# Optimization experiments

Measured on AMD Instinct MI355X. Metric: run time of the kernel, lower is better.

The kernel has to match this reference:

```python
import jax, jax.numpy as jnp
import numpy as np

SEQ, BATCH, HIDDEN = 2048, 2, 2048
NUM_HEADS = 16
HEAD_DIM = HIDDEN // NUM_HEADS  # 128


def setup_inputs() -> dict:
    key = jax.random.key(0)
    k1, k2, k3, k4, k5 = jax.random.split(key, 5)
    scale = 1.0 / np.sqrt(HIDDEN)
    return {
        "hidden_states": jax.random.normal(k1, (SEQ, BATCH, HIDDEN), dtype=jnp.float32),
        "w_qkv": jax.random.normal(k2, (3 * HIDDEN, HIDDEN), dtype=jnp.float32) * scale,
        "b_qkv": jax.random.normal(k3, (3 * HIDDEN,), dtype=jnp.float32) * 0.01,
        "w_dense": jax.random.normal(k4, (HIDDEN, HIDDEN), dtype=jnp.float32) * scale,
        "b_dense": jax.random.normal(k5, (HIDDEN,), dtype=jnp.float32) * 0.01,
    }


def reference(hidden_states, w_qkv, b_qkv, w_dense, b_dense):
    s, b, H = hidden_states.shape
    nh, d = NUM_HEADS, HEAD_DIM
    norm_factor = jnp.asarray(np.sqrt(d), dtype=hidden_states.dtype)

    # QKV projection: [s, b, 3H] -> [s, b, nh, 3d] -> chunk into q, k, v
    mixed = hidden_states @ w_qkv.T + b_qkv
    mixed = mixed.reshape(s, b, nh, 3 * d)
    q, k, v = jnp.split(mixed, 3, axis=-1)  # each [s, b, nh, d]

    # Causal scaled dot-product attention, materializing [b, nh, sq, sk]
    scores = jnp.einsum("sbhd,tbhd->bhst", q, k) / norm_factor
    causal = jnp.tril(jnp.ones((s, s), dtype=bool))  # [sq, sk]
    scores = jnp.where(causal[None, None, :, :], scores, jnp.asarray(-10000.0, scores.dtype))
    probs = jax.nn.softmax(scores, axis=-1)

    # Context: [s, b, nh, d] -> [s, b, H]
    ctx = jnp.einsum("bhst,tbhd->sbhd", probs, v).reshape(s, b, H)

    # Output projection
    return ctx @ w_dense.T + b_dense
```

## Files before the change

### kernel.cpp

```cpp
#include <hip/hip_runtime.h>
#include <stdint.h>
#include <stddef.h>

#define SEQ   2048
#define BATCH 2
#define HID   2048
#define NH    16
#define HD    128
#define MTOT  (SEQ*BATCH)
#define NQKV  (3*HID)
#define KDIM  HID
#define LOG2E 1.4426950408889634f

#define BK64    64
#define NT64    (KDIM/BK64)

typedef short  bf16x8 __attribute__((ext_vector_type(8)));
typedef float  f32x4  __attribute__((ext_vector_type(4)));

__device__ __forceinline__ unsigned short f2bf(float f) {
  union { float f; uint32_t u; } a; a.f = f;
  uint32_t r = a.u + 0x7fffu + ((a.u >> 16) & 1u);
  return (unsigned short)(r >> 16);
}

__device__ __forceinline__ f32x4 mfma16(bf16x8 a, bf16x8 b, f32x4 c) {
  return __builtin_amdgcn_mfma_f32_16x16x32_bf16(a, b, c, 0, 0, 0);
}

__device__ __forceinline__ void gl_lds16(const unsigned short* g, unsigned short* l) {
  __builtin_amdgcn_global_load_lds(
      (const __attribute__((address_space(1))) void*)g,
      (__attribute__((address_space(3))) void*)l, 16, 0, 0);
}

__global__ void cvt_f32_bf16(const float* __restrict__ in,
                             unsigned short* __restrict__ out, int n4) {
  int i = blockIdx.x * blockDim.x + threadIdx.x;
  int stride = gridDim.x * blockDim.x;
  for (; i < n4; i += stride) {
    float4 f = reinterpret_cast<const float4*>(in)[i];
    ushort4 o;
    o.x = f2bf(f.x); o.y = f2bf(f.y); o.z = f2bf(f.z); o.w = f2bf(f.w);
    reinterpret_cast<ushort4*>(out)[i] = o;
  }
}

__global__ __launch_bounds__(256) void transpose_v(
    const unsigned short* __restrict__ V, unsigned short* __restrict__ Vt) {
  __shared__ unsigned short tile[64][72];
  const int t  = threadIdx.x;
  const int bh = blockIdx.z;
  const int s0 = blockIdx.x * 64;
  const int d0 = blockIdx.y * 64;
  const size_t vb = (size_t)bh * SEQ * HD;
  const size_t tb = (size_t)bh * HD * SEQ;
#pragma unroll
  for (int p = 0; p < 2; ++p) {
    int r = p * 32 + (t >> 3);
    *(uint4*)&tile[r][(t & 7) * 8] =
        *(const uint4*)&V[vb + (size_t)(s0 + r) * HD + d0 + (t & 7) * 8];
  }
  __syncthreads();
#pragma unroll
  for (int p = 0; p < 2; ++p) {
    int dr = p * 32 + (t >> 3);
    int sc = (t & 7) * 8;
    unsigned short tmp[8];
#pragma unroll
    for (int e = 0; e < 8; ++e) tmp[e] = tile[sc + e][dr];
    *(uint4*)&Vt[tb + (size_t)(d0 + dr) * SEQ + s0 + sc] = *(const uint4*)tmp;
  }
}


#define G8_SB()  asm volatile("s_barrier" ::: "memory")
#define G8_LGKM() do { asm volatile("s_waitcnt lgkmcnt(0)" ::: "memory");     \
                       __builtin_amdgcn_sched_barrier(0); } while (0)

#define G8_RDA(G) do {                                                        \
    p0 = *(const bf16x8*)&sb[abase + (2*(G)    ) * 1024 + ga0];               \
    p1 = *(const bf16x8*)&sb[abase + (2*(G)    ) * 1024 + ga1];               \
    p2 = *(const bf16x8*)&sb[abase + (2*(G) + 1) * 1024 + ga0];               \
    p3 = *(const bf16x8*)&sb[abase + (2*(G) + 1) * 1024 + ga1];               \
  } while (0)

#define G8_MFMA(G) do {                                                       \
    __builtin_amdgcn_s_setprio(1);                                            \
    _Pragma("unroll")                                                         \
    for (int n_ = 0; n_ < 4; ++n_) {                                          \
      acc[2*(G)][n_]     = mfma16(p0, bq0[n_], acc[2*(G)][n_]);               \
      acc[2*(G)][n_]     = mfma16(p1, bq1[n_], acc[2*(G)][n_]);               \
      acc[2*(G) + 1][n_] = mfma16(p2, bq0[n_], acc[2*(G) + 1][n_]);           \
      acc[2*(G) + 1][n_] = mfma16(p3, bq1[n_], acc[2*(G) + 1][n_]);           \
    }                                                                         \
    __builtin_amdgcn_sched_barrier(0);                                        \
    __builtin_amdgcn_s_setprio(0);                                            \
  } while (0)

#define G8_STA(R) gl_lds16(Asrc + (size_t)(R) * KDIM + koff,                  \
                           &db[((R) + w * 8) * 64])
#define G8_STB(R) gl_lds16(Bsrc + (size_t)(R) * KDIM + koff,                  \
                           &db[16384 + ((R) + w * 8) * 64])

#define G8_TILE(DOSTAGE, VM1, VM3) do {                                       \
    bf16x8 bq0[4], bq1[4], p0, p1, p2, p3;                                    \
                                                       \
    _Pragma("unroll")                                                         \
    for (int n_ = 0; n_ < 4; ++n_) {                                          \
      bq0[n_] = *(const bf16x8*)&sb[bbase + n_ * 1024 + ga0];                 \
      bq1[n_] = *(const bf16x8*)&sb[bbase + n_ * 1024 + ga1];                 \
    }                                                                         \
    G8_RDA(0);                                                                \
    if (DOSTAGE) { G8_STB(0); G8_STB(64); }                                   \
    G8_SB(); G8_LGKM();                                                       \
    G8_MFMA(0);                                                               \
    G8_SB();                                                                  \
                                                       \
    G8_RDA(1);                                                                \
    if (DOSTAGE) { G8_STB(128); G8_STB(192); }                                \
    asm volatile("s_waitcnt " VM1 ::: "memory");                              \
    G8_SB(); G8_LGKM();                                                       \
    G8_MFMA(1);                                                               \
    G8_SB();                                                                  \
                                                       \
    G8_RDA(2);                                                                \
    if (DOSTAGE) { G8_STA(0); G8_STA(128); }                                  \
    G8_SB(); G8_LGKM();                                                       \
    G8_MFMA(2);                                                               \
    G8_SB();                                                                  \
                                                       \
    G8_RDA(3);                                                                \
    if (DOSTAGE) { G8_STA(64); G8_STA(192); }                                 \
    asm volatile("s_waitcnt " VM3 ::: "memory");                              \
    G8_SB(); G8_LGKM();                                                       \
    G8_MFMA(3);                                                               \
    G8_SB();                                                                  \
  } while (0)

__global__ __launch_bounds__(512, 2) void qkv_gemm(
    const unsigned short* __restrict__ A,
    const unsigned short* __restrict__ B,
    const float* __restrict__ bias,
    unsigned short* __restrict__ Qo,
    unsigned short* __restrict__ Ko,
    unsigned short* __restrict__ Vo)
{
  __shared__ unsigned short smb[2 * 32768];
  const int id  = blockIdx.x;
  const int swz = (id & 7) * 48 + (id >> 3);
  const int m0 = (swz / 24) * 256, n0 = (swz % 24) * 256;
  const int t = threadIdx.x, l = t & 63, w = t >> 6;
  const int wm = w >> 2, wn = w & 3;
  const int fr = l & 15, fg = l >> 4;
  const int abase = (wm * 128 + fr) * 64;
  const int bbase = 16384 + (wn * 64 + fr) * 64;
  const int ga0 = ((fg     ) ^ (fr & 7)) * 8;
  const int ga1 = ((fg + 4 ) ^ (fr & 7)) * 8;
  const int srcrow = w * 8 + (l >> 3);
  const int sgr    = ((l & 7) ^ (l >> 3)) * 8;
  const unsigned short* Asrc = A + (size_t)(m0 + srcrow) * KDIM + sgr;
  const unsigned short* Bsrc = B + (size_t)(n0 + srcrow) * KDIM + sgr;
  f32x4 acc[8][4] = {};

  {
    unsigned short* db = smb;
    size_t koff = 0;
    G8_STB(0); G8_STB(64); G8_STB(128); G8_STB(192);
    G8_STA(0); G8_STA(128); G8_STA(64); G8_STA(192);
  }
  asm volatile("s_waitcnt vmcnt(2)" ::: "memory");
  asm volatile("s_barrier" ::: "memory");

#pragma unroll 1
  for (int kt = 0; kt < NT64 - 1; ++kt) {
    const unsigned short* sb = &smb[(kt & 1) * 32768];
    unsigned short* db = &smb[((kt + 1) & 1) * 32768];
    size_t koff = (size_t)(kt + 1) * BK64;
    G8_TILE(1, "vmcnt(4)", "vmcnt(2)");
  }
  {
    const unsigned short* sb = &smb[((NT64 - 1) & 1) * 32768];
    unsigned short* db = smb;
    size_t koff = 0; (void)koff;
    G8_TILE(0, "vmcnt(0)", "vmcnt(0)");
  }

#pragma unroll
  for (int n = 0; n < 4; ++n) {
    int ncol = n0 + wn * 64 + n * 16 + fr;
    float bv = bias[ncol];
    int head = ncol / 384;
    int rem  = ncol - head * 384;
    int wi   = rem >> 7;
    int d    = rem & 127;
    unsigned short* dst = (wi == 0) ? Qo : ((wi == 1) ? Ko : Vo);
#pragma unroll
    for (int m = 0; m < 8; ++m) {
#pragma unroll
      for (int j = 0; j < 4; ++j) {
        int r = m0 + wm * 128 + m * 16 + fg * 4 + j;
        int s = r >> 1, bb = r & 1;
        float val = acc[m][n][j] + bv;
        if (wi == 0) val *= 0.08838834764831845f;
        dst[(((size_t)(bb * NH + head)) * SEQ + s) * HD + d] = f2bf(val);
      }
    }
  }
}


#define GEMM_PRE()                                                            \
  const int t = threadIdx.x, l = t & 63, w = t >> 6;                          \
  const int wm = w >> 1, wn = w & 1;                                          \
  const int fr = l & 15, fg = l >> 4;                                         \
  const int fx = fr & 7;                                                      \
  const int srow = l >> 3;                                                    \
  const int sgr  = ((l & 7) ^ srow) * 8;                                      \
  const unsigned short* Aw = A + (size_t)(m0 + w * 32 + srow) * KDIM + sgr;   \
  const unsigned short* Bw = B + (size_t)(n0 + w * 16 + srow) * KDIM + sgr;   \
  unsigned short* smb = &sm[0][0];                                            \
  const int a0 = (wm * 64 + fr) * 64 + ((fg ^ fx) * 8);                       \
  const int a1 = (wm * 64 + fr) * 64 + (((4 + fg) ^ fx) * 8);                 \
  const int b0 = 16384 + (wn * 64 + fr) * 64 + ((fg ^ fx) * 8);               \
  const int b1 = 16384 + (wn * 64 + fr) * 64 + (((4 + fg) ^ fx) * 8);         \
  f32x4 acc[4][4] = {};

#define STAGE_AB(KT) do {                                                     \
    unsigned short* dst = &smb[((KT) % 3) * 24576];                           \
    const unsigned short* ap = Aw + (size_t)(KT) * BK64;                      \
    gl_lds16(ap,                    &dst[(w * 4 + 0) * 512]);                 \
    gl_lds16(ap + 8  * KDIM,        &dst[(w * 4 + 1) * 512]);                 \
    gl_lds16(ap + 16 * KDIM,        &dst[(w * 4 + 2) * 512]);                 \
    gl_lds16(ap + 24 * KDIM,        &dst[(w * 4 + 3) * 512]);                 \
    const unsigned short* bp = Bw + (size_t)(KT) * BK64;                      \
    gl_lds16(bp,                    &dst[16384 + (w * 2 + 0) * 512]);         \
    gl_lds16(bp + 8 * KDIM,         &dst[16384 + (w * 2 + 1) * 512]);         \
  } while (0)

#define GEMM_BODY(KT, VM, DOSTAGE) do {                                       \
    const unsigned short* sb = &smb[((KT) % 3) * 24576];                      \
    if (DOSTAGE) STAGE_AB((KT) + 2);                                          \
    bf16x8 af0[4], af1[4], bg0[4], bg1[4];                                    \
    _Pragma("unroll")                                                         \
    for (int m_ = 0; m_ < 4; ++m_) {                                          \
      af0[m_] = *(const bf16x8*)&sb[a0 + m_ * 1024];                          \
      af1[m_] = *(const bf16x8*)&sb[a1 + m_ * 1024];                          \
    }                                                                         \
    _Pragma("unroll")                                                         \
    for (int n_ = 0; n_ < 4; ++n_) {                                          \
      bg0[n_] = *(const bf16x8*)&sb[b0 + n_ * 1024];                          \
      bg1[n_] = *(const bf16x8*)&sb[b1 + n_ * 1024];                          \
    }                                                                         \
    asm volatile("s_waitcnt vmcnt(" #VM ")" ::: "memory");                    \
    asm volatile("s_barrier" ::: "memory");                                   \
    asm volatile("s_waitcnt lgkmcnt(0)" ::: "memory");                        \
    __builtin_amdgcn_sched_barrier(0);                                        \
    __builtin_amdgcn_s_setprio(1);                                            \
    _Pragma("unroll")                                                         \
    for (int m_ = 0; m_ < 4; ++m_)                                            \
      _Pragma("unroll")                                                       \
      for (int n_ = 0; n_ < 4; ++n_)                                          \
        acc[m_][n_] = mfma16(af0[m_], bg0[n_], acc[m_][n_]);                  \
    _Pragma("unroll")                                                         \
    for (int m_ = 0; m_ < 4; ++m_)                                            \
      _Pragma("unroll")                                                       \
      for (int n_ = 0; n_ < 4; ++n_)                                          \
        acc[m_][n_] = mfma16(af1[m_], bg1[n_], acc[m_][n_]);                  \
    __builtin_amdgcn_sched_barrier(0);                                        \
    __builtin_amdgcn_s_setprio(0);                                            \
    asm volatile("s_barrier" ::: "memory");                                   \
  } while (0)

#define GEMM_MAIN()                                                           \
  STAGE_AB(0); STAGE_AB(1);                                                   \
  asm volatile("s_waitcnt vmcnt(6)" ::: "memory");                            \
  asm volatile("s_barrier" ::: "memory");                                     \
  _Pragma("unroll 1")                                                         \
  for (int kt = 0; kt < NT64 - 2; ++kt)                                       \
    GEMM_BODY(kt, 6, 1);                                                      \
  GEMM_BODY(NT64 - 2, 0, 0);                                                  \
  GEMM_BODY(NT64 - 1, 0, 0);

__global__ __launch_bounds__(512, 1) void dense_gemm(
    const unsigned short* __restrict__ A,
    const unsigned short* __restrict__ B,
    const float* __restrict__ bias,
    float* __restrict__ out)
{
  __shared__ unsigned short sm[3][24576];
  int id  = blockIdx.x;
  int swz = (id & 7) * (gridDim.x >> 3) + (id >> 3);
  const int m0 = (swz / 16) * 256, n0 = (swz % 16) * 128;
  GEMM_PRE();
  GEMM_MAIN();

  const int g4 = fg * 4;
#pragma unroll
  for (int n = 0; n < 4; ++n) {
    int ncol = n0 + wn * 64 + n * 16 + fr;
    float bv = bias[ncol];
#pragma unroll
    for (int m = 0; m < 4; ++m) {
#pragma unroll
      for (int j = 0; j < 4; ++j) {
        int r = m0 + wm * 64 + m * 16 + g4 + j;
        out[(size_t)r * HID + ncol] = acc[m][n][j] + bv;
      }
    }
  }
}

__global__ __launch_bounds__(256, 2) void attn_fwd(
    const unsigned short* __restrict__ Q,
    const unsigned short* __restrict__ K,
    const unsigned short* __restrict__ Vt,
    unsigned short* __restrict__ ctx)
{
  __shared__ unsigned short Ksh[2][64 * 128];
  __shared__ unsigned short Vsh[2][128 * 64];
  __shared__ unsigned short Psh[4][16 * 72];
  const int t = threadIdx.x, l = t & 63, w = t >> 6;
  int nwg = gridDim.x * gridDim.y;
  int id  = blockIdx.y * gridDim.x + blockIdx.x;
  int swz = (id & 7) * (nwg >> 3) + (id >> 3);
  const int pair = swz & 15;
  const int bh   = swz >> 4;
  const int qtA = pair, qtB = 31 - pair;
  const int fr = l & 15, fg = l >> 4;
  const size_t base  = (size_t)bh * SEQ * HD;
  const size_t vbase = (size_t)bh * HD * SEQ;

#define STAGE(BUF, KT) do {                                                   \
    const unsigned short* Kt_ = K + base + (size_t)((KT) * 64) * HD;          \
    _Pragma("unroll")                                                         \
    for (int i_ = 0; i_ < 4; ++i_) {                                          \
      int ch_  = w * 4 + i_;                                                  \
      int row_ = ch_ * 4 + (l >> 4);                                          \
      int c16_ = (l & 15) ^ (row_ & 7);                                       \
      gl_lds16(Kt_ + (size_t)row_ * HD + c16_ * 8, &Ksh[BUF][ch_ * 512]);     \
    }                                                                         \
    const unsigned short* Vg_ = Vt + vbase + (KT) * 64;                       \
    _Pragma("unroll")                                                         \
    for (int i_ = 0; i_ < 4; ++i_) {                                          \
      int ch_  = w * 4 + i_;                                                  \
      int row_ = ch_ * 8 + (l >> 3);                                          \
      int c16_ = (l & 7) ^ (row_ & 7);                                        \
      gl_lds16(Vg_ + (size_t)row_ * SEQ + c16_ * 8, &Vsh[BUF][ch_ * 512]);    \
    }                                                                         \
  } while (0)

#define COMPUTE_TILE(QF, OACC, MROW, LROW, QT) do {                           \
    f32x4 sacc[4] = {};                                                       \
    _Pragma("unroll")                                                         \
    for (int c_ = 0; c_ < 4; ++c_) {                                          \
      _Pragma("unroll")                                                       \
      for (int n_ = 0; n_ < 4; ++n_) {                                        \
        int krow = n_ * 16 + fr;                                              \
        int g_   = (c_ * 4 + fg) ^ (krow & 7);                                \
        bf16x8 kf = *(const bf16x8*)&Ksh[buf][krow * 128 + g_ * 8];           \
        sacc[n_] = mfma16(QF[c_], kf, sacc[n_]);                              \
      }                                                                       \
    }                                                                         \
    if (kt == (QT)) {                                                         \
      _Pragma("unroll")                                                       \
      for (int n_ = 0; n_ < 4; ++n_)                                          \
        _Pragma("unroll")                                                     \
        for (int j_ = 0; j_ < 4; ++j_)                                        \
          if (n_ * 16 + fr > w * 16 + fg * 4 + j_) sacc[n_][j_] = -1e30f;     \
    }                                                                         \
    float tm_[4];                                                             \
    _Pragma("unroll")                                                         \
    for (int j_ = 0; j_ < 4; ++j_) {                                          \
      float v0 = fmaxf(fmaxf(sacc[0][j_], sacc[1][j_]),                       \
                       fmaxf(sacc[2][j_], sacc[3][j_]));                      \
      v0 = fmaxf(v0, __shfl_xor(v0, 1));                                      \
      v0 = fmaxf(v0, __shfl_xor(v0, 2));                                      \
      v0 = fmaxf(v0, __shfl_xor(v0, 4));                                      \
      v0 = fmaxf(v0, __shfl_xor(v0, 8));                                      \
      tm_[j_] = v0;                                                           \
    }                                                                         \
    float sc_[4], ps_[4];                                                     \
    _Pragma("unroll")                                                         \
    for (int j_ = 0; j_ < 4; ++j_) {                                          \
      float mn_ = fmaxf(MROW[j_], tm_[j_]);                                   \
      sc_[j_] = exp2f((MROW[j_] - mn_) * LOG2E);                              \
      MROW[j_] = mn_;                                                         \
      ps_[j_] = 0.f;                                                          \
    }                                                                         \
    _Pragma("unroll")                                                         \
    for (int n_ = 0; n_ < 4; ++n_)                                            \
      _Pragma("unroll")                                                       \
      for (int j_ = 0; j_ < 4; ++j_) {                                        \
        float p_ = exp2f((sacc[n_][j_] - MROW[j_]) * LOG2E);                  \
        sacc[n_][j_] = p_;                                                    \
        ps_[j_] += p_;                                                        \
      }                                                                       \
    _Pragma("unroll")                                                         \
    for (int j_ = 0; j_ < 4; ++j_) {                                          \
      float s_ = ps_[j_];                                                     \
      s_ += __shfl_xor(s_, 1);                                                \
      s_ += __shfl_xor(s_, 2);                                                \
      s_ += __shfl_xor(s_, 4);                                                \
      s_ += __shfl_xor(s_, 8);                                                \
      LROW[j_] = LROW[j_] * sc_[j_] + s_;                                     \
    }                                                                         \
    _Pragma("unroll")                                                         \
    for (int n_ = 0; n_ < 8; ++n_)                                            \
      _Pragma("unroll")                                                       \
      for (int j_ = 0; j_ < 4; ++j_)                                          \
        OACC[n_][j_] *= sc_[j_];                                              \
    _Pragma("unroll")                                                         \
    for (int n_ = 0; n_ < 4; ++n_)                                            \
      _Pragma("unroll")                                                       \
      for (int j_ = 0; j_ < 4; ++j_)                                          \
        Psh[w][(fg * 4 + j_) * 72 + n_ * 16 + fr] = f2bf(sacc[n_][j_]);       \
    _Pragma("unroll")                                                         \
    for (int ks_ = 0; ks_ < 2; ++ks_) {                                       \
      bf16x8 pf = *(const bf16x8*)&Psh[w][fr * 72 + ks_ * 32 + fg * 8];       \
      _Pragma("unroll")                                                       \
      for (int n_ = 0; n_ < 8; ++n_) {                                        \
        int vrow = n_ * 16 + fr;                                              \
        int g_   = (ks_ * 4 + fg) ^ (vrow & 7);                               \
        bf16x8 vf = *(const bf16x8*)&Vsh[buf][vrow * 64 + g_ * 8];            \
        OACC[n_] = mfma16(pf, vf, OACC[n_]);                                  \
      }                                                                       \
    }                                                                         \
  } while (0)

  bf16x8 qfA[4], qfB[4];
  {
    const unsigned short* qpA = Q + base + (size_t)(qtA * 64 + w * 16 + fr) * HD + fg * 8;
    const unsigned short* qpB = Q + base + (size_t)(qtB * 64 + w * 16 + fr) * HD + fg * 8;
#pragma unroll
    for (int c = 0; c < 4; ++c) {
      qfA[c] = *(const bf16x8*)(qpA + c * 32);
      qfB[c] = *(const bf16x8*)(qpB + c * 32);
    }
  }
  f32x4 oaccA[8] = {}, oaccB[8] = {};
  float mA[4] = {-1e30f, -1e30f, -1e30f, -1e30f};
  float mB[4] = {-1e30f, -1e30f, -1e30f, -1e30f};
  float lA[4] = {0.f, 0.f, 0.f, 0.f};
  float lB[4] = {0.f, 0.f, 0.f, 0.f};

  STAGE(0, 0);
  __syncthreads();
  int buf = 0;
  for (int kt = 0; kt <= qtB; ++kt) {
    if (kt < qtB) STAGE(buf ^ 1, kt + 1);
    COMPUTE_TILE(qfB, oaccB, mB, lB, qtB);
    if (kt <= qtA) COMPUTE_TILE(qfA, oaccA, mA, lA, qtA);
    __syncthreads();
    buf ^= 1;
  }

  const int bb = bh >> 4, h = bh & 15;
#define WRITE_CTX(OACC, LROW, QT) do {                                        \
    _Pragma("unroll")                                                         \
    for (int n_ = 0; n_ < 8; ++n_)                                            \
      _Pragma("unroll")                                                       \
      for (int j_ = 0; j_ < 4; ++j_) {                                        \
        int qrow = (QT) * 64 + w * 16 + fg * 4 + j_;                          \
        float val = OACC[n_][j_] / LROW[j_];                                  \
        ctx[((size_t)(qrow * BATCH + bb)) * HID + h * HD + n_ * 16 + fr] =    \
            f2bf(val);                                                        \
      }                                                                       \
  } while (0)
  WRITE_CTX(oaccA, lA, qtA);
  WRITE_CTX(oaccB, lB, qtB);
#undef STAGE
#undef COMPUTE_TILE
#undef WRITE_CTX
}

extern "C" void kernel_launch(void* const* d_in, const int* in_sizes, int n_in,
                              void* d_out, int out_size, void* d_ws, size_t ws_size,
                              hipStream_t stream) {
  const float* hs      = (const float*)d_in[0];
  const float* w_qkv   = (const float*)d_in[1];
  const float* b_qkv   = (const float*)d_in[2];
  const float* w_dense = (const float*)d_in[3];
  const float* b_dense = (const float*)d_in[4];
  float* out = (float*)d_out;

  unsigned short* hsb = (unsigned short*)d_ws;
  unsigned short* wqb = hsb + (size_t)MTOT * HID;
  unsigned short* wdb = wqb + (size_t)NQKV * HID;
  unsigned short* q   = wdb + (size_t)HID * HID;
  unsigned short* k   = q   + (size_t)MTOT * HID;
  unsigned short* v   = k   + (size_t)MTOT * HID;
  unsigned short* ctx = v   + (size_t)MTOT * HID;
  unsigned short* vt  = hsb;

  cvt_f32_bf16<<<2048, 256, 0, stream>>>(hs,      hsb, (MTOT * HID) / 4);
  cvt_f32_bf16<<<2048, 256, 0, stream>>>(w_qkv,   wqb, (NQKV * HID) / 4);
  cvt_f32_bf16<<<1024, 256, 0, stream>>>(w_dense, wdb, (HID * HID) / 4);

  qkv_gemm<<<dim3((MTOT / 256) * (NQKV / 256)), 512, 0, stream>>>(hsb, wqb, b_qkv, q, k, v);
  transpose_v<<<dim3(SEQ / 64, HD / 64, BATCH * NH), 256, 0, stream>>>(v, vt);
  attn_fwd<<<dim3(16, 32), 256, 0, stream>>>(q, k, vt, ctx);
  dense_gemm<<<dim3((MTOT / 256) * (HID / 128)), 512, 0, stream>>>(ctx, wdb, b_dense, out);
}
```

Baseline: 285.4 us.

## Retile QKV GEMM to 256x192 blocks and merge conversion kernels

The QKV GEMM tile shrinks from 256x256 to 256x192. The grid grows from 384 to 512 blocks, which matches the CU count better (256 CUs with 2 blocks each) and avoids a partial wave. LDS staging, the swizzle and the per-wave MFMA loops are adjusted so each wave covers 48 columns, and the global-to-LDS stage ordering is rebalanced. The three f32-to-bf16 conversion launches are merged into one kernel to cut launch overhead. The trade-off is lower arithmetic intensity per block and changed vmcnt accounting in the pipeline.

After: 275.0 us. 1.04x faster.

```diff
diff --git a/kernel.cpp b/kernel.cpp
--- a/kernel.cpp
+++ b/kernel.cpp
@@ -34,15 +34,21 @@
       (__attribute__((address_space(3))) void*)l, 16, 0, 0);
 }
 
-__global__ void cvt_f32_bf16(const float* __restrict__ in,
-                             unsigned short* __restrict__ out, int n4) {
+__global__ void cvt3_f32_bf16(const float* __restrict__ a, unsigned short* __restrict__ oa, int na,
+                              const float* __restrict__ b, unsigned short* __restrict__ ob, int nb,
+                              const float* __restrict__ c, unsigned short* __restrict__ oc, int nc) {
   int i = blockIdx.x * blockDim.x + threadIdx.x;
   int stride = gridDim.x * blockDim.x;
-  for (; i < n4; i += stride) {
-    float4 f = reinterpret_cast<const float4*>(in)[i];
+  int ntot = na + nb + nc;
+  for (; i < ntot; i += stride) {
+    const float* src; unsigned short* dst; int j;
+    if (i < na)           { src = a; dst = oa; j = i; }
+    else if (i < na + nb) { src = b; dst = ob; j = i - na; }
+    else                  { src = c; dst = oc; j = i - na - nb; }
+    float4 f = reinterpret_cast<const float4*>(src)[j];
     ushort4 o;
     o.x = f2bf(f.x); o.y = f2bf(f.y); o.z = f2bf(f.z); o.w = f2bf(f.w);
-    reinterpret_cast<ushort4*>(out)[i] = o;
+    reinterpret_cast<ushort4*>(dst)[j] = o;
   }
 }
 
@@ -74,6 +80,8 @@
 }
 
 
+#define QBUFS 28672
+
 #define G8_SB()  asm volatile("s_barrier" ::: "memory")
 #define G8_LGKM() do { asm volatile("s_waitcnt lgkmcnt(0)" ::: "memory");     \
                        __builtin_amdgcn_sched_barrier(0); } while (0)
@@ -88,7 +96,7 @@
 #define G8_MFMA(G) do {                                                       \
     __builtin_amdgcn_s_setprio(1);                                            \
     _Pragma("unroll")                                                         \
-    for (int n_ = 0; n_ < 4; ++n_) {                                          \
+    for (int n_ = 0; n_ < 3; ++n_) {                                          \
       acc[2*(G)][n_]     = mfma16(p0, bq0[n_], acc[2*(G)][n_]);               \
       acc[2*(G)][n_]     = mfma16(p1, bq1[n_], acc[2*(G)][n_]);               \
       acc[2*(G) + 1][n_] = mfma16(p2, bq0[n_], acc[2*(G) + 1][n_]);           \
@@ -104,10 +112,10 @@
                            &db[16384 + ((R) + w * 8) * 64])
 
 #define G8_TILE(DOSTAGE, VM1, VM3) do {                                       \
-    bf16x8 bq0[4], bq1[4], p0, p1, p2, p3;                                    \
+    bf16x8 bq0[3], bq1[3], p0, p1, p2, p3;                                    \
                                                        \
     _Pragma("unroll")                                                         \
-    for (int n_ = 0; n_ < 4; ++n_) {                                          \
+    for (int n_ = 0; n_ < 3; ++n_) {                                          \
       bq0[n_] = *(const bf16x8*)&sb[bbase + n_ * 1024 + ga0];                 \
       bq1[n_] = *(const bf16x8*)&sb[bbase + n_ * 1024 + ga1];                 \
     }                                                                         \
@@ -118,20 +126,20 @@
     G8_SB();                                                                  \
                                                        \
     G8_RDA(1);                                                                \
-    if (DOSTAGE) { G8_STB(128); G8_STB(192); }                                \
+    if (DOSTAGE) { G8_STB(128); G8_STA(0); }                                  \
     asm volatile("s_waitcnt " VM1 ::: "memory");                              \
     G8_SB(); G8_LGKM();                                                       \
     G8_MFMA(1);                                                               \
     G8_SB();                                                                  \
                                                        \
     G8_RDA(2);                                                                \
-    if (DOSTAGE) { G8_STA(0); G8_STA(128); }                                  \
+    if (DOSTAGE) { G8_STA(128); G8_STA(64); }                                 \
     G8_SB(); G8_LGKM();                                                       \
     G8_MFMA(2);                                                               \
     G8_SB();                                                                  \
                                                        \
     G8_RDA(3);                                                                \
-    if (DOSTAGE) { G8_STA(64); G8_STA(192); }                                 \
+    if (DOSTAGE) { G8_STA(192); }                                             \
     asm volatile("s_waitcnt " VM3 ::: "memory");                              \
     G8_SB(); G8_LGKM();                                                       \
     G8_MFMA(3);                                                               \
@@ -146,27 +154,27 @@
     unsigned short* __restrict__ Ko,
     unsigned short* __restrict__ Vo)
 {
-  __shared__ unsigned short smb[2 * 32768];
+  __shared__ unsigned short smb[2 * QBUFS];
   const int id  = blockIdx.x;
-  const int swz = (id & 7) * 48 + (id >> 3);
-  const int m0 = (swz / 24) * 256, n0 = (swz % 24) * 256;
+  const int swz = (id & 7) * 64 + (id >> 3);
+  const int m0 = (swz >> 5) * 256, n0 = (swz & 31) * 192;
   const int t = threadIdx.x, l = t & 63, w = t >> 6;
   const int wm = w >> 2, wn = w & 3;
   const int fr = l & 15, fg = l >> 4;
   const int abase = (wm * 128 + fr) * 64;
-  const int bbase = 16384 + (wn * 64 + fr) * 64;
+  const int bbase = 16384 + (wn * 48 + fr) * 64;
   const int ga0 = ((fg     ) ^ (fr & 7)) * 8;
   const int ga1 = ((fg + 4 ) ^ (fr & 7)) * 8;
   const int srcrow = w * 8 + (l >> 3);
   const int sgr    = ((l & 7) ^ (l >> 3)) * 8;
   const unsigned short* Asrc = A + (size_t)(m0 + srcrow) * KDIM + sgr;
   const unsigned short* Bsrc = B + (size_t)(n0 + srcrow) * KDIM + sgr;
-  f32x4 acc[8][4] = {};
+  f32x4 acc[8][3] = {};
 
   {
     unsigned short* db = smb;
     size_t koff = 0;
-    G8_STB(0); G8_STB(64); G8_STB(128); G8_STB(192);
+    G8_STB(0); G8_STB(64); G8_STB(128);
     G8_STA(0); G8_STA(128); G8_STA(64); G8_STA(192);
   }
   asm volatile("s_waitcnt vmcnt(2)" ::: "memory");
@@ -174,21 +182,21 @@
 
 #pragma unroll 1
   for (int kt = 0; kt < NT64 - 1; ++kt) {
-    const unsigned short* sb = &smb[(kt & 1) * 32768];
-    unsigned short* db = &smb[((kt + 1) & 1) * 32768];
+    const unsigned short* sb = &smb[(kt & 1) * QBUFS];
+    unsigned short* db = &smb[((kt + 1) & 1) * QBUFS];
     size_t koff = (size_t)(kt + 1) * BK64;
     G8_TILE(1, "vmcnt(4)", "vmcnt(2)");
   }
   {
-    const unsigned short* sb = &smb[((NT64 - 1) & 1) * 32768];
+    const unsigned short* sb = &smb[((NT64 - 1) & 1) * QBUFS];
     unsigned short* db = smb;
     size_t koff = 0; (void)koff;
     G8_TILE(0, "vmcnt(0)", "vmcnt(0)");
   }
 
 #pragma unroll
-  for (int n = 0; n < 4; ++n) {
-    int ncol = n0 + wn * 64 + n * 16 + fr;
+  for (int n = 0; n < 3; ++n) {
+    int ncol = n0 + wn * 48 + n * 16 + fr;
     float bv = bias[ncol];
     int head = ncol / 384;
     int rem  = ncol - head * 384;
@@ -493,11 +501,12 @@
   unsigned short* ctx = v   + (size_t)MTOT * HID;
   unsigned short* vt  = hsb;
 
-  cvt_f32_bf16<<<2048, 256, 0, stream>>>(hs,      hsb, (MTOT * HID) / 4);
-  cvt_f32_bf16<<<2048, 256, 0, stream>>>(w_qkv,   wqb, (NQKV * HID) / 4);
-  cvt_f32_bf16<<<1024, 256, 0, stream>>>(w_dense, wdb, (HID * HID) / 4);
-
-  qkv_gemm<<<dim3((MTOT / 256) * (NQKV / 256)), 512, 0, stream>>>(hsb, wqb, b_qkv, q, k, v);
+  cvt3_f32_bf16<<<2048, 256, 0, stream>>>(
+      hs, hsb, (MTOT * HID) / 4,
+      w_qkv, wqb, (NQKV * HID) / 4,
+      w_dense, wdb, (HID * HID) / 4);
+
+  qkv_gemm<<<dim3((MTOT / 256) * (NQKV / 192)), 512, 0, stream>>>(hsb, wqb, b_qkv, q, k, v);
   transpose_v<<<dim3(SEQ / 64, HD / 64, BATCH * NH), 256, 0, stream>>>(v, vt);
   attn_fwd<<<dim3(16, 32), 256, 0, stream>>>(q, k, vt, ctx);
   dense_gemm<<<dim3((MTOT / 256) * (HID / 128)), 512, 0, stream>>>(ctx, wdb, b_dense, out);
```
